# Optimization experiments

Hardware: AMD Instinct MI355X
Metric: run time of the kernel (lower is better)

Reference implementation:

```python
import jax, jax.numpy as jnp
import numpy as np

B, S, D = 2, 1024, 1024
E = 8          # routed experts
I = 1024       # per-expert intermediate
IS = 1024      # shared expert intermediate
TOP_K = 2
NUM_SHARED = 1


def setup_inputs() -> dict:
    key = jax.random.key(0)
    ks = jax.random.split(key, 8)
    scale = 0.02
    return {
        "x": jax.random.normal(ks[0], (B, S, D), dtype=jnp.float32),
        "w_gate": jax.random.normal(ks[1], (D, E), dtype=jnp.float32) * scale,
        "wg": jax.random.normal(ks[2], (E, D, I), dtype=jnp.float32) * scale,  # expert gate_proj
        "wu": jax.random.normal(ks[3], (E, D, I), dtype=jnp.float32) * scale,  # expert up_proj
        "wd": jax.random.normal(ks[4], (E, I, D), dtype=jnp.float32) * scale,  # expert down_proj
        "ws_g": jax.random.normal(ks[5], (NUM_SHARED, D, IS), dtype=jnp.float32) * scale,
        "ws_u": jax.random.normal(ks[6], (NUM_SHARED, D, IS), dtype=jnp.float32) * scale,
        "ws_d": jax.random.normal(ks[7], (NUM_SHARED, IS, D), dtype=jnp.float32) * scale,
    }


def _swiglu(t, w_gate_proj, w_up, w_down):
    # t: [N, D]
    g = t @ w_gate_proj            # [N, I]
    u = t @ w_up                   # [N, I]
    return (jax.nn.silu(g) * u) @ w_down  # [N, D]


def reference(x, w_gate, wg, wu, wd, ws_g, ws_u, ws_d):
    Bb, Ss, Dd = x.shape
    x_flat = x.reshape(Bb * Ss, Dd)                  # [N, D]
    N = x_flat.shape[0]

    # --- router ---
    logits = x_flat @ w_gate                          # [N, E]
    topk_logits, topk_idx = jax.lax.top_k(logits, TOP_K)
    topk_w = jax.nn.softmax(topk_logits, axis=-1)     # [N, K]

    # --- aux load-balancing loss ---
    one_hot = jax.nn.one_hot(topk_idx, E, dtype=jnp.float32)  # [N, K, E]
    f = one_hot.sum(axis=1).mean(axis=0)                       # [E]
    P = jax.nn.softmax(logits, axis=-1).mean(axis=0)           # [E]
    aux_loss = E * jnp.sum(f * P)

    # --- combine weights: cw[n, e] = sum_k topk_w[n,k] * 1[topk_idx[n,k]==e] ---
    cw = jnp.einsum("nk,nke->ne", topk_w, one_hot)             # [N, E]

    # --- routed experts: dense compute over all experts, weighted combine ---
    g = jnp.einsum("nd,edi->eni", x_flat, wg)                  # [E, N, I]
    u = jnp.einsum("nd,edi->eni", x_flat, wu)                  # [E, N, I]
    a = jax.nn.silu(g) * u                                     # [E, N, I]
    y = jnp.einsum("eni,eid->end", a, wd)                      # [E, N, D]
    routed = jnp.einsum("ne,end->nd", cw, y)                   # [N, D]

    # --- shared experts ---
    shared = jnp.zeros_like(x_flat)
    for s in range(NUM_SHARED):
        shared = shared + _swiglu(x_flat, ws_g[s], ws_u[s], ws_d[s])

    out = (routed + shared).reshape(Bb, Ss, Dd)
    return out, aux_loss
```

## Files before the change

kernel.cpp:

```cpp
#include <hip/hip_runtime.h>
#include <math.h>

typedef unsigned short u16;
typedef __attribute__((ext_vector_type(8))) short short8;
typedef __attribute__((ext_vector_type(4))) float f32x4;
typedef __attribute__((ext_vector_type(4))) unsigned short u16x4;
typedef __attribute__((ext_vector_type(8))) unsigned short u16x8;

#define N_TOK 2048
#define DIM 1024
#define OUT_ELEMS 2097152

#define GLDS16(gp, lp) __builtin_amdgcn_global_load_lds( \
    (const __attribute__((address_space(1))) unsigned int*)(gp), \
    (__attribute__((address_space(3))) unsigned int*)(lp), 16, 0, 0)

__device__ __forceinline__ u16 f2bf(float f) {
    union { float f; unsigned u; } v; v.f = f;
    unsigned r = (v.u + 0x7FFFu + ((v.u >> 16) & 1u)) >> 16;
    return (u16)r;
}
__device__ __forceinline__ float bf2f(u16 h) {
    union { unsigned u; float f; } v; v.u = ((unsigned)h) << 16;
    return v.f;
}

__device__ __forceinline__ void cvt_chunk(const float* __restrict__ src,
                                          u16* __restrict__ dst, int chunk,
                                          char* smem, int t) {
    float* tile = (float*)smem;
    const char* gsrc = (const char*)(src + (size_t)chunk * 8192);
    u16* dchunk = dst + (size_t)chunk * 8192;
    int w = t >> 6, l = t & 63;
#pragma unroll
    for (int j = 0; j < 8; j++) {
        int idx = w * 8 + j;
        GLDS16(gsrc + idx * 1024 + l * 16, smem + idx * 1024);
    }
    __syncthreads();
    int n0 = (t & 63) * 4 + (t >> 6) * 256;
    f32x4 v[8];
#pragma unroll
    for (int k = 0; k < 8; k++)
        v[k] = *(const f32x4*)(tile + k * 1024 + n0);
#pragma unroll
    for (int i = 0; i < 4; i++) {
        u16x8 o;
#pragma unroll
        for (int k = 0; k < 8; k++) o[k] = f2bf(v[k][i]);
        *(u16x8*)(dchunk + (size_t)(n0 + i) * 8) = o;
    }
}

__device__ __forceinline__ void cvt_gu_job(int j, const float* wg, const float* wu,
                                           const float* wsg, const float* wsu,
                                           u16* wgt, u16* wut, u16* wsgt, u16* wsut,
                                           char* smem, int t) {
    int mat = j >> 7, chunk = j & 127;
    const float* src; u16* dst;
    if      (mat <  8) { src = wg + (size_t)mat * 1048576;       dst = wgt + (size_t)mat * 1048576; }
    else if (mat < 16) { src = wu + (size_t)(mat - 8) * 1048576; dst = wut + (size_t)(mat - 8) * 1048576; }
    else if (mat == 16){ src = wsg; dst = wsgt; }
    else               { src = wsu; dst = wsut; }
    cvt_chunk(src, dst, chunk, smem, t);
}

__device__ __forceinline__ void cvt_d_job(int j, const float* wd, const float* wsd,
                                          u16* wdt, u16* wsdt, char* smem, int t) {
    int mat = j >> 7, chunk = j & 127;
    const float* src = (mat < 8) ? (wd + (size_t)mat * 1048576) : wsd;
    u16* dst = (mat < 8) ? (wdt + (size_t)mat * 1048576) : wsdt;
    cvt_chunk(src, dst, chunk, smem, t);
}

__device__ __forceinline__ void router_job(int b, const float* x, const float* wgate,
                                           u16* xb, int* tidx, float* tw,
                                           float* Pp, int* Cp, int* tlist,
                                           int* curs, char* smem, int t) {
    float* sP = (float*)smem;
    int*   sC = (int*)(smem + 64);
    if (t < 8) { sP[t] = 0.f; sC[t] = 0; }
    if (b == 0 && t < 16) curs[t] = 0;
    __syncthreads();
    int wave = t >> 6;
    int lane = t & 63;
    int n = b * 4 + wave;
    const float* xr = x + (size_t)n * DIM;
    u16* xbr = xb + (size_t)n * DIM;
    float acc[8] = {0.f,0.f,0.f,0.f,0.f,0.f,0.f,0.f};
#pragma unroll
    for (int i = 0; i < 16; i++) {
        int d = lane + i * 64;
        float xv = xr[d];
        xbr[d] = f2bf(xv);
        const float* wr = wgate + d * 8;
#pragma unroll
        for (int e = 0; e < 8; e++) acc[e] += xv * wr[e];
    }
#pragma unroll
    for (int off = 32; off; off >>= 1) {
#pragma unroll
        for (int e = 0; e < 8; e++) acc[e] += __shfl_xor(acc[e], off);
    }
    if (lane == 0) {
        tlist[4096 + n] = n;
        float mx = acc[0];
#pragma unroll
        for (int e = 1; e < 8; e++) mx = fmaxf(mx, acc[e]);
        float p[8], s = 0.f;
#pragma unroll
        for (int e = 0; e < 8; e++) { p[e] = expf(acc[e] - mx); s += p[e]; }
        float inv = 1.f / s;
#pragma unroll
        for (int e = 0; e < 8; e++) atomicAdd(&sP[e], p[e] * inv);
        int i0 = 0; float b0 = acc[0];
#pragma unroll
        for (int e = 1; e < 8; e++) if (acc[e] > b0) { b0 = acc[e]; i0 = e; }
        int i1 = -1; float b1 = -3.4e38f;
#pragma unroll
        for (int e = 0; e < 8; e++) if (e != i0 && acc[e] > b1) { b1 = acc[e]; i1 = e; }
        float w0 = 1.f / (1.f + expf(b1 - b0));
        tidx[n * 2] = i0; tidx[n * 2 + 1] = i1;
        tw[n * 2] = w0;   tw[n * 2 + 1] = 1.f - w0;
        atomicAdd(&sC[i0], 1);
        atomicAdd(&sC[i1], 1);
    }
    __syncthreads();
    if (t < 8) { Pp[b * 8 + t] = sP[t]; Cp[b * 8 + t] = sC[t]; }
}

__device__ __forceinline__ void scatter_job(int bid, const int* tidx, const float* Pp,
                                            const int* Cp, int* curs, int* tlist,
                                            int* slots, float* out, int* counts,
                                            int* offs, char* smem, int t) {
    int*   s_off = (int*)smem;
    int*   sCnt  = (int*)(smem + 32);
    float* sPs   = (float*)(smem + 64);
    int*   redC  = (int*)(smem + 128);
    float* redP  = (float*)(smem + 1152);
    int e = t & 7, g = t >> 3;
    int cs = 0; float ps = 0.f;
#pragma unroll
    for (int j = 0; j < 16; j++) {
        int b = g + j * 32;
        cs += Cp[b * 8 + e];
        ps += Pp[b * 8 + e];
    }
    redC[t] = cs; redP[t] = ps;
    __syncthreads();
    if (t < 8) {
        int c = 0; float p = 0.f;
        for (int g2 = 0; g2 < 32; g2++) { c += redC[g2 * 8 + t]; p += redP[g2 * 8 + t]; }
        sCnt[t] = c; sPs[t] = p;
    }
    __syncthreads();
    if (t == 0) {
        int o = 0;
        for (int e2 = 0; e2 < 8; e2++) { s_off[e2] = o; o += sCnt[e2]; }
    }
    __syncthreads();
    if (bid == 0 && t == 0) {
        float aux = 0.f;
        for (int e2 = 0; e2 < 8; e2++) {
            aux += (float)sCnt[e2] * sPs[e2];
            offs[e2] = s_off[e2]; counts[e2] = sCnt[e2];
        }
        out[OUT_ELEMS] = 8.f * aux / ((float)N_TOK * (float)N_TOK);
        offs[8] = 4096; counts[8] = 2048;
    }
    int n = bid * 256 + t;
    if (n < N_TOK) {
#pragma unroll
        for (int k = 0; k < 2; k++) {
            int ee = tidx[n * 2 + k];
            int p = atomicAdd(&curs[ee], 1);
            int sl = s_off[ee] + p;
            tlist[sl] = n;
            slots[n * 2 + k] = sl;
        }
    }
}

__device__ __forceinline__ void gemm_map(int jj, int& job, int& mt, int& nt) {
    if (jj < 128) { job = 8; mt = jj >> 3; nt = jj & 7; }
    else {
        int r = jj - 128;
        mt = r >> 6;
        int rem = r & 63;
        job = rem >> 3;
        nt = rem & 7;
    }
}

__device__ __forceinline__ void gemm1_job(
    int jj, const u16* __restrict__ xb, const u16* __restrict__ wgt,
    const u16* __restrict__ wut, const u16* __restrict__ wsgt,
    const u16* __restrict__ wsut, const int* __restrict__ tlist,
    const int* __restrict__ counts, const int* __restrict__ offs,
    u16* __restrict__ H, char* smem, int t) {
    int job, mt, nt; gemm_map(jj, job, mt, nt);
    int jcnt = counts[job];
    int m0 = mt << 7;
    if (m0 >= jcnt) return;
    int joff = offs[job];
    int n0 = nt << 7;
    const u16* Bg = (job < 8) ? (wgt + (size_t)job * 1048576) : wsgt;
    const u16* Bu = (job < 8) ? (wut + (size_t)job * 1048576) : wsut;

    int wave = t >> 6, lane = t & 63;
    int ch = (lane & 3) * 8;
    int r0 = (wave * 2 + 0) * 16 + (lane >> 2);
    int r1 = (wave * 2 + 1) * 16 + (lane >> 2);
    int tok0 = tlist[joff + m0 + r0];
    int tok1 = tlist[joff + m0 + r1];
    const u16* a0 = xb + (size_t)tok0 * 1024 + ch;
    const u16* a1 = xb + (size_t)tok1 * 1024 + ch;
    const u16* gB = Bg + (size_t)wave * 8192 + (size_t)(n0 + lane) * 8;
    const u16* uB = Bu + (size_t)wave * 8192 + (size_t)(n0 + lane) * 8;

    int wm = (wave >> 1) << 6, wn = (wave & 1) << 6;
    int quad = lane >> 4, lr = lane & 15;

    f32x4 accg[4][4], accu[4][4];
    f32x4 zz = {0.f, 0.f, 0.f, 0.f};
#pragma unroll
    for (int i = 0; i < 4; i++)
#pragma unroll
        for (int j = 0; j < 4; j++) { accg[i][j] = zz; accu[i][j] = zz; }

#define STAGE1(b_, s_) do { \
        char* bb = smem + (b_) * 24576; \
        u16* As_  = (u16*)bb; \
        u16* Bgs_ = (u16*)(bb + 8192); \
        u16* Bus_ = (u16*)(bb + 16384); \
        int k0_ = (s_) * 32; \
        size_t koff_ = (size_t)k0_ * 1024; \
        GLDS16(a0 + k0_, As_ + (wave * 2 + 0) * 512); \
        GLDS16(a1 + k0_, As_ + (wave * 2 + 1) * 512); \
        GLDS16(gB + koff_,       Bgs_ + wave * 1024); \
        GLDS16(gB + koff_ + 512, Bgs_ + wave * 1024 + 512); \
        GLDS16(uB + koff_,       Bus_ + wave * 1024); \
        GLDS16(uB + koff_ + 512, Bus_ + wave * 1024 + 512); \
    } while (0)

    STAGE1(0, 0);
    __syncthreads();
    for (int s = 0; s < 32; s++) {
        int cur = s & 1;
        if (s < 31) STAGE1(cur ^ 1, s + 1);
        const char* cb = smem + cur * 24576;
        const u16* Asr = (const u16*)cb;
        const u16* Bgr = (const u16*)(cb + 8192);
        const u16* Bur = (const u16*)(cb + 16384);
        short8 af[4], bgf[4], buf[4];
#pragma unroll
        for (int i = 0; i < 4; i++) {
            int nrow = wn + i * 16 + lr;
            af[i]  = *(const short8*)(Asr + (wm + i * 16 + lr) * 32 + quad * 8);
            bgf[i] = *(const short8*)(Bgr + quad * 1024 + nrow * 8);
            buf[i] = *(const short8*)(Bur + quad * 1024 + nrow * 8);
        }
#pragma unroll
        for (int mi = 0; mi < 4; mi++)
#pragma unroll
            for (int ni = 0; ni < 4; ni++) {
                accg[mi][ni] = __builtin_amdgcn_mfma_f32_16x16x32_bf16(af[mi], bgf[ni], accg[mi][ni], 0, 0, 0);
                accu[mi][ni] = __builtin_amdgcn_mfma_f32_16x16x32_bf16(af[mi], buf[ni], accu[mi][ni], 0, 0, 0);
            }
        __syncthreads();
    }
#undef STAGE1
#pragma unroll
    for (int mi = 0; mi < 4; mi++) {
        int rowb = m0 + wm + mi * 16 + quad * 4;
#pragma unroll
        for (int rr = 0; rr < 4; rr++) {
            int row = rowb + rr;
            if (row < jcnt) {
                size_t base = (size_t)(joff + row) * 1024 + n0 + wn;
#pragma unroll
                for (int ni = 0; ni < 4; ni++) {
                    float g = accg[mi][ni][rr];
                    float u = accu[mi][ni][rr];
                    float h = (g / (1.f + expf(-g))) * u;
                    H[base + ni * 16 + lr] = f2bf(h);
                }
            }
        }
    }
}

__device__ __forceinline__ void gemm2_job(
    int jj, const u16* __restrict__ H, const u16* __restrict__ wdt,
    const u16* __restrict__ wsdt, const int* __restrict__ counts,
    const int* __restrict__ offs, u16* __restrict__ Y, char* smem, int t) {
    int job, mt, nt; gemm_map(jj, job, mt, nt);
    int jcnt = counts[job];
    int m0 = mt << 7;
    if (m0 >= jcnt) return;
    int joff = offs[job];
    int n0 = nt << 7;
    const u16* Bt = (job < 8) ? (wdt + (size_t)job * 1048576) : wsdt;

    int wave = t >> 6, lane = t & 63;
    int ch = (lane & 3) * 8;
    int r0 = (wave * 2 + 0) * 16 + (lane >> 2);
    int r1 = (wave * 2 + 1) * 16 + (lane >> 2);
    const u16* a0 = H + (size_t)(joff + m0 + r0) * 1024 + ch;
    const u16* a1 = H + (size_t)(joff + m0 + r1) * 1024 + ch;
    const u16* bB = Bt + (size_t)wave * 8192 + (size_t)(n0 + lane) * 8;

    int wm = (wave >> 1) << 6, wn = (wave & 1) << 6;
    int quad = lane >> 4, lr = lane & 15;

    f32x4 acc[4][4];
    f32x4 zz = {0.f, 0.f, 0.f, 0.f};
#pragma unroll
    for (int i = 0; i < 4; i++)
#pragma unroll
        for (int j = 0; j < 4; j++) acc[i][j] = zz;

#define STAGE2(b_, s_) do { \
        char* bb = smem + (b_) * 16384; \
        u16* As_ = (u16*)bb; \
        u16* Bs_ = (u16*)(bb + 8192); \
        int k0_ = (s_) * 32; \
        size_t koff_ = (size_t)k0_ * 1024; \
        GLDS16(a0 + k0_, As_ + (wave * 2 + 0) * 512); \
        GLDS16(a1 + k0_, As_ + (wave * 2 + 1) * 512); \
        GLDS16(bB + koff_,       Bs_ + wave * 1024); \
        GLDS16(bB + koff_ + 512, Bs_ + wave * 1024 + 512); \
    } while (0)

    STAGE2(0, 0);
    __syncthreads();
    for (int s = 0; s < 32; s++) {
        int cur = s & 1;
        if (s < 31) STAGE2(cur ^ 1, s + 1);
        const char* cb = smem + cur * 16384;
        const u16* Asr = (const u16*)cb;
        const u16* Bsr = (const u16*)(cb + 8192);
        short8 af[4], bf[4];
#pragma unroll
        for (int i = 0; i < 4; i++) {
            af[i] = *(const short8*)(Asr + (wm + i * 16 + lr) * 32 + quad * 8);
            bf[i] = *(const short8*)(Bsr + quad * 1024 + (wn + i * 16 + lr) * 8);
        }
#pragma unroll
        for (int mi = 0; mi < 4; mi++)
#pragma unroll
            for (int ni = 0; ni < 4; ni++)
                acc[mi][ni] = __builtin_amdgcn_mfma_f32_16x16x32_bf16(af[mi], bf[ni], acc[mi][ni], 0, 0, 0);
        __syncthreads();
    }
#undef STAGE2
#pragma unroll
    for (int mi = 0; mi < 4; mi++) {
        int rowb = m0 + wm + mi * 16 + quad * 4;
#pragma unroll
        for (int rr = 0; rr < 4; rr++) {
            int row = rowb + rr;
            if (row < jcnt) {
                u16* yrow = Y + (size_t)(joff + row) * 1024 + n0 + wn;
#pragma unroll
                for (int ni = 0; ni < 4; ni++)
                    yrow[ni * 16 + lr] = f2bf(acc[mi][ni][rr]);
            }
        }
    }
}

__device__ __forceinline__ void combine_job(int n, const u16* __restrict__ Y,
                                            const int* __restrict__ slots,
                                            const float* __restrict__ tw,
                                            float* __restrict__ out, int t) {
    int s0 = slots[n * 2], s1 = slots[n * 2 + 1];
    float w0 = tw[n * 2], w1 = tw[n * 2 + 1];
    u16x4 y0 = ((const u16x4*)(Y + (size_t)s0 * 1024))[t];
    u16x4 y1 = ((const u16x4*)(Y + (size_t)s1 * 1024))[t];
    u16x4 ys = ((const u16x4*)(Y + (size_t)(4096 + n) * 1024))[t];
    f32x4 r;
    r.x = w0 * bf2f(y0.x) + w1 * bf2f(y1.x) + bf2f(ys.x);
    r.y = w0 * bf2f(y0.y) + w1 * bf2f(y1.y) + bf2f(ys.y);
    r.z = w0 * bf2f(y0.z) + w1 * bf2f(y1.z) + bf2f(ys.z);
    r.w = w0 * bf2f(y0.w) + w1 * bf2f(y1.w) + bf2f(ys.w);
    ((f32x4*)(out + (size_t)n * 1024))[t] = r;
}

__global__ __launch_bounds__(256)
void k_front(const float* __restrict__ wg, const float* __restrict__ wu,
             const float* __restrict__ wsg, const float* __restrict__ wsu,
             u16* __restrict__ wgt, u16* __restrict__ wut,
             u16* __restrict__ wsgt, u16* __restrict__ wsut,
             const float* __restrict__ x, const float* __restrict__ wgate,
             u16* __restrict__ xb, int* __restrict__ tidx, float* __restrict__ tw,
             float* __restrict__ Pp, int* __restrict__ Cp,
             int* __restrict__ tlist, int* __restrict__ curs) {
    __shared__ __attribute__((aligned(128))) char smem[32768];
    int bx = blockIdx.x, t = threadIdx.x;
    if (bx < 512) router_job(bx, x, wgate, xb, tidx, tw, Pp, Cp, tlist, curs, smem, t);
    else          cvt_gu_job(bx - 512, wg, wu, wsg, wsu, wgt, wut, wsgt, wsut, smem, t);
}

__global__ void k_scatter(const int* __restrict__ tidx, const float* __restrict__ Pp,
                          const int* __restrict__ Cp, int* __restrict__ curs,
                          int* __restrict__ tlist, int* __restrict__ slots,
                          float* __restrict__ out, int* __restrict__ counts,
                          int* __restrict__ offs) {
    __shared__ __attribute__((aligned(128))) char smem[4096];
    scatter_job(blockIdx.x, tidx, Pp, Cp, curs, tlist, slots, out, counts, offs,
                smem, threadIdx.x);
}

__global__ __launch_bounds__(256, 2)
void k_gemm1(const u16* __restrict__ xb, const u16* __restrict__ wgt,
             const u16* __restrict__ wut, const u16* __restrict__ wsgt,
             const u16* __restrict__ wsut, const int* __restrict__ tlist,
             const int* __restrict__ counts, const int* __restrict__ offs,
             u16* __restrict__ H,
             const float* __restrict__ wd, const float* __restrict__ wsd,
             u16* __restrict__ wdt, u16* __restrict__ wsdt) {
    __shared__ __attribute__((aligned(128))) char smem[49152];
    int bx = blockIdx.x, t = threadIdx.x;
    if (bx < 1152) gemm1_job(bx, xb, wgt, wut, wsgt, wsut, tlist, counts, offs, H, smem, t);
    else           cvt_d_job(bx - 1152, wd, wsd, wdt, wsdt, smem, t);
}

__global__ __launch_bounds__(256, 2)
void k_gemm2(const u16* __restrict__ H, const u16* __restrict__ wdt,
             const u16* __restrict__ wsdt, const int* __restrict__ counts,
             const int* __restrict__ offs, u16* __restrict__ Y) {
    __shared__ __attribute__((aligned(128))) char smem[32768];
    gemm2_job(blockIdx.x, H, wdt, wsdt, counts, offs, Y, smem, threadIdx.x);
}

__global__ void k_combine(const u16* __restrict__ Y, const int* __restrict__ slots,
                          const float* __restrict__ tw, float* __restrict__ out) {
    combine_job(blockIdx.x, Y, slots, tw, out, threadIdx.x);
}

extern "C" void kernel_launch(void* const* d_in, const int* in_sizes, int n_in,
                              void* d_out, int out_size, void* d_ws, size_t ws_size,
                              hipStream_t stream) {
    const float* x     = (const float*)d_in[0];
    const float* wgate = (const float*)d_in[1];
    const float* wg    = (const float*)d_in[2];
    const float* wu    = (const float*)d_in[3];
    const float* wd    = (const float*)d_in[4];
    const float* wsg   = (const float*)d_in[5];
    const float* wsu   = (const float*)d_in[6];
    const float* wsd   = (const float*)d_in[7];
    float* out = (float*)d_out;

    char* ws = (char*)d_ws;
    u16*   xb    = (u16*)(ws + 0);
    u16*   wgt   = (u16*)(ws + 4194304);
    u16*   wut   = (u16*)(ws + 20971520);
    u16*   wdt   = (u16*)(ws + 37748736);
    u16*   wsgt  = (u16*)(ws + 54525952);
    u16*   wsut  = (u16*)(ws + 56623104);
    u16*   wsdt  = (u16*)(ws + 58720256);
    u16*   H     = (u16*)(ws + 60817408);
    u16*   Y     = (u16*)(ws + 4194304);
    int*   tidx  = (int*)(ws + 73400320);
    float* tw    = (float*)(ws + 73416704);
    int*   tlist = (int*)(ws + 73433088);
    int*   slots = (int*)(ws + 73457664);
    int*   counts= (int*)(ws + 73474048);
    int*   offs  = (int*)(ws + 73474112);
    int*   curs  = (int*)(ws + 73474176);
    float* Pp    = (float*)(ws + 73474304);
    int*   Cp    = (int*)(ws + 73490688);

    k_front<<<2816, 256, 0, stream>>>(wg, wu, wsg, wsu, wgt, wut, wsgt, wsut,
                                      x, wgate, xb, tidx, tw, Pp, Cp, tlist, curs);
    k_scatter<<<8, 256, 0, stream>>>(tidx, Pp, Cp, curs, tlist, slots,
                                     out, counts, offs);
    k_gemm1<<<2304, 256, 0, stream>>>(xb, wgt, wut, wsgt, wsut, tlist, counts, offs,
                                      H, wd, wsd, wdt, wsdt);
    k_gemm2<<<1152, 256, 0, stream>>>(H, wdt, wsdt, counts, offs, Y);
    k_combine<<<2048, 256, 0, stream>>>(Y, slots, tw, out);
}
```

Before: 239.9 us.

## Use 512-thread blocks for expert GEMMs with 32x64 per-wave tiles

Doubles the workgroup size of both expert GEMM kernels from 4 to 8 waves while keeping the 128x128 block tile. Each wave now owns a 32x64 sub-tile, so per-wave accumulators are halved. The global-to-LDS staging loads are respread so each wave issues fewer loads, with gate and up B-tiles split across wave groups. The down-weight conversion chunk is rewritten for 512 threads. The aim is more waves per CU and lower register pressure to hide latency, at the cost of more A/B fragment reloads from LDS per MFMA and heavier barriers.

```diff
diff --git a/kernel.cpp b/kernel.cpp
--- a/kernel.cpp
+++ b/kernel.cpp
@@ -48,6 +48,33 @@
         u16x8 o;
 #pragma unroll
         for (int k = 0; k < 8; k++) o[k] = f2bf(v[k][i]);
+        *(u16x8*)(dchunk + (size_t)(n0 + i) * 8) = o;
+    }
+}
+
+__device__ __forceinline__ void cvt_chunk512(const float* __restrict__ src,
+                                             u16* __restrict__ dst, int chunk,
+                                             char* smem, int t) {
+    float* tile = (float*)smem;
+    const char* gsrc = (const char*)(src + (size_t)chunk * 8192);
+    u16* dchunk = dst + (size_t)chunk * 8192;
+    int w = t >> 6, l = t & 63;
+#pragma unroll
+    for (int j = 0; j < 4; j++) {
+        int idx = w * 4 + j;
+        GLDS16(gsrc + idx * 1024 + l * 16, smem + idx * 1024);
+    }
+    __syncthreads();
+    int n0 = (t & 63) * 2 + (t >> 6) * 128;
+    float2 v[8];
+#pragma unroll
+    for (int k = 0; k < 8; k++)
+        v[k] = *(const float2*)(tile + k * 1024 + n0);
+#pragma unroll
+    for (int i = 0; i < 2; i++) {
+        u16x8 o;
+#pragma unroll
+        for (int k = 0; k < 8; k++) o[k] = f2bf(i ? v[k].y : v[k].x);
         *(u16x8*)(dchunk + (size_t)(n0 + i) * 8) = o;
     }
 }
@@ -65,12 +92,12 @@
     cvt_chunk(src, dst, chunk, smem, t);
 }
 
-__device__ __forceinline__ void cvt_d_job(int j, const float* wd, const float* wsd,
-                                          u16* wdt, u16* wsdt, char* smem, int t) {
+__device__ __forceinline__ void cvt_d_job512(int j, const float* wd, const float* wsd,
+                                             u16* wdt, u16* wsdt, char* smem, int t) {
     int mat = j >> 7, chunk = j & 127;
     const float* src = (mat < 8) ? (wd + (size_t)mat * 1048576) : wsd;
     u16* dst = (mat < 8) ? (wdt + (size_t)mat * 1048576) : wsdt;
-    cvt_chunk(src, dst, chunk, smem, t);
+    cvt_chunk512(src, dst, chunk, smem, t);
 }
 
 __device__ __forceinline__ void router_job(int b, const float* x, const float* wgate,
@@ -208,39 +235,32 @@
     const u16* Bu = (job < 8) ? (wut + (size_t)job * 1048576) : wsut;
 
     int wave = t >> 6, lane = t & 63;
-    int ch = (lane & 3) * 8;
-    int r0 = (wave * 2 + 0) * 16 + (lane >> 2);
-    int r1 = (wave * 2 + 1) * 16 + (lane >> 2);
-    int tok0 = tlist[joff + m0 + r0];
-    int tok1 = tlist[joff + m0 + r1];
-    const u16* a0 = xb + (size_t)tok0 * 1024 + ch;
-    const u16* a1 = xb + (size_t)tok1 * 1024 + ch;
-    const u16* gB = Bg + (size_t)wave * 8192 + (size_t)(n0 + lane) * 8;
-    const u16* uB = Bu + (size_t)wave * 8192 + (size_t)(n0 + lane) * 8;
-
-    int wm = (wave >> 1) << 6, wn = (wave & 1) << 6;
+    int arow = wave * 16 + (lane >> 2);
+    int tok = tlist[joff + m0 + arow];
+    const u16* aA = xb + (size_t)tok * 1024 + (lane & 3) * 8;
+    int cwv = wave & 3;
+    const u16* pB = ((wave < 4) ? Bg : Bu) + (size_t)cwv * 8192
+                  + (size_t)(n0 + lane) * 8;
+    int bOff = ((wave < 4) ? 8192 : 16384) + cwv * 2048;
+
+    int wm = (wave >> 1) << 5;
+    int wn = (wave & 1) << 6;
     int quad = lane >> 4, lr = lane & 15;
 
-    f32x4 accg[4][4], accu[4][4];
+    f32x4 accg[2][4], accu[2][4];
     f32x4 zz = {0.f, 0.f, 0.f, 0.f};
 #pragma unroll
-    for (int i = 0; i < 4; i++)
+    for (int i = 0; i < 2; i++)
 #pragma unroll
         for (int j = 0; j < 4; j++) { accg[i][j] = zz; accu[i][j] = zz; }
 
 #define STAGE1(b_, s_) do { \
         char* bb = smem + (b_) * 24576; \
-        u16* As_  = (u16*)bb; \
-        u16* Bgs_ = (u16*)(bb + 8192); \
-        u16* Bus_ = (u16*)(bb + 16384); \
         int k0_ = (s_) * 32; \
         size_t koff_ = (size_t)k0_ * 1024; \
-        GLDS16(a0 + k0_, As_ + (wave * 2 + 0) * 512); \
-        GLDS16(a1 + k0_, As_ + (wave * 2 + 1) * 512); \
-        GLDS16(gB + koff_,       Bgs_ + wave * 1024); \
-        GLDS16(gB + koff_ + 512, Bgs_ + wave * 1024 + 512); \
-        GLDS16(uB + koff_,       Bus_ + wave * 1024); \
-        GLDS16(uB + koff_ + 512, Bus_ + wave * 1024 + 512); \
+        GLDS16(aA + k0_, (u16*)bb + wave * 512); \
+        GLDS16(pB + koff_,       (u16*)(bb + bOff)); \
+        GLDS16(pB + koff_ + 512, (u16*)(bb + bOff + 1024)); \
     } while (0)
 
     STAGE1(0, 0);
@@ -252,16 +272,18 @@
         const u16* Asr = (const u16*)cb;
         const u16* Bgr = (const u16*)(cb + 8192);
         const u16* Bur = (const u16*)(cb + 16384);
-        short8 af[4], bgf[4], buf[4];
+        short8 af[2], bgf[4], buf[4];
+#pragma unroll
+        for (int i = 0; i < 2; i++)
+            af[i] = *(const short8*)(Asr + (wm + i * 16 + lr) * 32 + quad * 8);
 #pragma unroll
         for (int i = 0; i < 4; i++) {
             int nrow = wn + i * 16 + lr;
-            af[i]  = *(const short8*)(Asr + (wm + i * 16 + lr) * 32 + quad * 8);
             bgf[i] = *(const short8*)(Bgr + quad * 1024 + nrow * 8);
             buf[i] = *(const short8*)(Bur + quad * 1024 + nrow * 8);
         }
 #pragma unroll
-        for (int mi = 0; mi < 4; mi++)
+        for (int mi = 0; mi < 2; mi++)
 #pragma unroll
             for (int ni = 0; ni < 4; ni++) {
                 accg[mi][ni] = __builtin_amdgcn_mfma_f32_16x16x32_bf16(af[mi], bgf[ni], accg[mi][ni], 0, 0, 0);
@@ -271,7 +293,7 @@
     }
 #undef STAGE1
 #pragma unroll
-    for (int mi = 0; mi < 4; mi++) {
+    for (int mi = 0; mi < 2; mi++) {
         int rowb = m0 + wm + mi * 16 + quad * 4;
 #pragma unroll
         for (int rr = 0; rr < 4; rr++) {
@@ -303,33 +325,29 @@
     const u16* Bt = (job < 8) ? (wdt + (size_t)job * 1048576) : wsdt;
 
     int wave = t >> 6, lane = t & 63;
-    int ch = (lane & 3) * 8;
-    int r0 = (wave * 2 + 0) * 16 + (lane >> 2);
-    int r1 = (wave * 2 + 1) * 16 + (lane >> 2);
-    const u16* a0 = H + (size_t)(joff + m0 + r0) * 1024 + ch;
-    const u16* a1 = H + (size_t)(joff + m0 + r1) * 1024 + ch;
-    const u16* bB = Bt + (size_t)wave * 8192 + (size_t)(n0 + lane) * 8;
-
-    int wm = (wave >> 1) << 6, wn = (wave & 1) << 6;
+    int arow = wave * 16 + (lane >> 2);
+    const u16* aA = H + (size_t)(joff + m0 + arow) * 1024 + (lane & 3) * 8;
+    int cwv = wave >> 1, half = wave & 1;
+    const u16* pB = Bt + (size_t)cwv * 8192 + (size_t)(n0 + half * 64 + lane) * 8;
+    int bOff = 8192 + cwv * 2048 + half * 1024;
+
+    int wm = (wave >> 1) << 5;
+    int wn = (wave & 1) << 6;
     int quad = lane >> 4, lr = lane & 15;
 
-    f32x4 acc[4][4];
+    f32x4 acc[2][4];
     f32x4 zz = {0.f, 0.f, 0.f, 0.f};
 #pragma unroll
-    for (int i = 0; i < 4; i++)
+    for (int i = 0; i < 2; i++)
 #pragma unroll
         for (int j = 0; j < 4; j++) acc[i][j] = zz;
 
 #define STAGE2(b_, s_) do { \
         char* bb = smem + (b_) * 16384; \
-        u16* As_ = (u16*)bb; \
-        u16* Bs_ = (u16*)(bb + 8192); \
         int k0_ = (s_) * 32; \
         size_t koff_ = (size_t)k0_ * 1024; \
-        GLDS16(a0 + k0_, As_ + (wave * 2 + 0) * 512); \
-        GLDS16(a1 + k0_, As_ + (wave * 2 + 1) * 512); \
-        GLDS16(bB + koff_,       Bs_ + wave * 1024); \
-        GLDS16(bB + koff_ + 512, Bs_ + wave * 1024 + 512); \
+        GLDS16(aA + k0_, (u16*)bb + wave * 512); \
+        GLDS16(pB + koff_, (u16*)(bb + bOff)); \
     } while (0)
 
     STAGE2(0, 0);
@@ -340,14 +358,15 @@
         const char* cb = smem + cur * 16384;
         const u16* Asr = (const u16*)cb;
         const u16* Bsr = (const u16*)(cb + 8192);
-        short8 af[4], bf[4];
-#pragma unroll
-        for (int i = 0; i < 4; i++) {
+        short8 af[2], bf[4];
+#pragma unroll
+        for (int i = 0; i < 2; i++)
             af[i] = *(const short8*)(Asr + (wm + i * 16 + lr) * 32 + quad * 8);
+#pragma unroll
+        for (int i = 0; i < 4; i++)
             bf[i] = *(const short8*)(Bsr + quad * 1024 + (wn + i * 16 + lr) * 8);
-        }
-#pragma unroll
-        for (int mi = 0; mi < 4; mi++)
+#pragma unroll
+        for (int mi = 0; mi < 2; mi++)
 #pragma unroll
             for (int ni = 0; ni < 4; ni++)
                 acc[mi][ni] = __builtin_amdgcn_mfma_f32_16x16x32_bf16(af[mi], bf[ni], acc[mi][ni], 0, 0, 0);
@@ -355,7 +374,7 @@
     }
 #undef STAGE2
 #pragma unroll
-    for (int mi = 0; mi < 4; mi++) {
+    for (int mi = 0; mi < 2; mi++) {
         int rowb = m0 + wm + mi * 16 + quad * 4;
 #pragma unroll
         for (int rr = 0; rr < 4; rr++) {
@@ -412,7 +431,7 @@
                 smem, threadIdx.x);
 }
 
-__global__ __launch_bounds__(256, 2)
+__global__ __launch_bounds__(512, 2)
 void k_gemm1(const u16* __restrict__ xb, const u16* __restrict__ wgt,
              const u16* __restrict__ wut, const u16* __restrict__ wsgt,
              const u16* __restrict__ wsut, const int* __restrict__ tlist,
@@ -423,10 +442,10 @@
     __shared__ __attribute__((aligned(128))) char smem[49152];
     int bx = blockIdx.x, t = threadIdx.x;
     if (bx < 1152) gemm1_job(bx, xb, wgt, wut, wsgt, wsut, tlist, counts, offs, H, smem, t);
-    else           cvt_d_job(bx - 1152, wd, wsd, wdt, wsdt, smem, t);
-}
-
-__global__ __launch_bounds__(256, 2)
+    else           cvt_d_job512(bx - 1152, wd, wsd, wdt, wsdt, smem, t);
+}
+
+__global__ __launch_bounds__(512, 2)
 void k_gemm2(const u16* __restrict__ H, const u16* __restrict__ wdt,
              const u16* __restrict__ wsdt, const int* __restrict__ counts,
              const int* __restrict__ offs, u16* __restrict__ Y) {
@@ -476,8 +495,8 @@
                                       x, wgate, xb, tidx, tw, Pp, Cp, tlist, curs);
     k_scatter<<<8, 256, 0, stream>>>(tidx, Pp, Cp, curs, tlist, slots,
                                      out, counts, offs);
-    k_gemm1<<<2304, 256, 0, stream>>>(xb, wgt, wut, wsgt, wsut, tlist, counts, offs,
+    k_gemm1<<<2304, 512, 0, stream>>>(xb, wgt, wut, wsgt, wsut, tlist, counts, offs,
                                       H, wd, wsd, wdt, wsdt);
-    k_gemm2<<<1152, 256, 0, stream>>>(H, wdt, wsdt, counts, offs, Y);
+    k_gemm2<<<1152, 512, 0, stream>>>(H, wdt, wsdt, counts, offs, Y);
     k_combine<<<2048, 256, 0, stream>>>(Y, slots, tw, out);
 }
```

Result: no change. 235.8 us (-1.7%).
